# Optimization experiments

Measured on AMD Instinct MI355X. Metric: run time of the kernel, lower is better.

The kernel has to match this reference:

```python
import jax, jax.numpy as jnp
import numpy as np

D_MODEL = 1024
NUM_HEADS = 16
D_K = D_MODEL // NUM_HEADS
THETA = 10000.0


def setup_inputs() -> dict:
    key = jax.random.key(0)
    ks = jax.random.split(key, 5)
    B, S = 2, 2048
    sigma = np.sqrt(2.0 / (D_MODEL + D_MODEL))
    x = jax.random.normal(ks[0], (B, S, D_MODEL), dtype=jnp.float32)
    Wq = jax.random.normal(ks[1], (D_MODEL, D_MODEL), dtype=jnp.float32) * sigma
    Wk = jax.random.normal(ks[2], (D_MODEL, D_MODEL), dtype=jnp.float32) * sigma
    Wv = jax.random.normal(ks[3], (D_MODEL, D_MODEL), dtype=jnp.float32) * sigma
    Wo = jax.random.normal(ks[4], (D_MODEL, D_MODEL), dtype=jnp.float32) * sigma
    return {"x": x, "Wq": Wq, "Wk": Wk, "Wv": Wv, "Wo": Wo}


def _rope(x, cos, sin):
    # x: [B, H, S, D_K]; cos/sin: [S, D_K//2] broadcast to [1, 1, S, D_K//2]
    x1 = x[..., ::2]
    x2 = x[..., 1::2]
    even = x1 * cos - x2 * sin
    odd = x1 * sin + x2 * cos
    return jnp.stack((even, odd), axis=-1).reshape(x.shape)


def reference(x, Wq, Wk, Wv, Wo):
    B, S, _ = x.shape
    # projections: weight is (out, in), applied as einsum('oi,...i->...o')
    q = jnp.einsum('oi,bsi->bso', Wq, x).reshape(B, S, NUM_HEADS, D_K).transpose(0, 2, 1, 3)
    k = jnp.einsum('oi,bsi->bso', Wk, x).reshape(B, S, NUM_HEADS, D_K).transpose(0, 2, 1, 3)
    v = jnp.einsum('oi,bsi->bso', Wv, x).reshape(B, S, NUM_HEADS, D_K).transpose(0, 2, 1, 3)
    # RoPE tables (token_positions = arange(S))
    inv_freq = 1.0 / (THETA ** (jnp.arange(0, D_K, 2, dtype=jnp.float32) / D_K))
    t = jnp.arange(S, dtype=jnp.float32)
    freqs = t[:, None] * inv_freq[None, :]          # [S, D_K/2]
    cos = jnp.cos(freqs)[None, None]                # [1,1,S,D_K/2]
    sin = jnp.sin(freqs)[None, None]
    q = _rope(q, cos, sin)
    k = _rope(k, cos, sin)
    # causal attention, full materialized scores (faithful to source)
    scores = jnp.einsum('bhid,bhjd->bhij', q, k) / np.sqrt(D_K).astype(np.float32)
    causal = jnp.tril(jnp.ones((S, S), dtype=bool))
    scores = jnp.where(causal, scores, -jnp.inf)
    attn = jax.nn.softmax(scores, axis=-1)
    out = jnp.einsum('bhij,bhjd->bhid', attn, v)    # [B,H,S,D_K]
    out = out.transpose(0, 2, 1, 3).reshape(B, S, D_MODEL)
    return jnp.einsum('oi,bsi->bso', Wo, out)
```

## Files before the change

kernel.cpp:

```cpp
#include <hip/hip_runtime.h>

#define D_MODEL 1024
#define NUM_HEADS 16
#define SEQ 2048
#define BATCH 2

typedef __attribute__((ext_vector_type(8))) short bf16x8;
typedef __attribute__((ext_vector_type(4))) float f32x4;

__device__ __forceinline__ float bf2f(unsigned short u) {
    return __uint_as_float(((unsigned int)u) << 16);
}
__device__ __forceinline__ unsigned short f2bf(float f) {
    unsigned int u = __float_as_uint(f);
    return (unsigned short)((u + 0x7FFFu + ((u >> 16) & 1u)) >> 16);
}
__device__ __forceinline__ ushort4 pack4(float4 v) {
    return make_ushort4(f2bf(v.x), f2bf(v.y), f2bf(v.z), f2bf(v.w));
}

__device__ __forceinline__ void gload_lds16(const unsigned short* g, unsigned short* l) {
    __builtin_amdgcn_global_load_lds(
        (const __attribute__((address_space(1))) unsigned int*)g,
        (__attribute__((address_space(3))) unsigned int*)l,
        16, 0, 0);
}

__device__ __forceinline__ bf16x8 lds_read_swz(const unsigned short (*tile)[64], int row, int chunk) {
    const char* p = reinterpret_cast<const char*>(tile);
    return *reinterpret_cast<const bf16x8*>(p + row * 128 + (((chunk ^ (row & 7))) << 4));
}

__device__ __forceinline__ bf16x8 lds_read_swz32(const unsigned short (*tile)[32], int row, int chunk) {
    const char* p = reinterpret_cast<const char*>(tile);
    return *reinterpret_cast<const bf16x8*>(p + row * 64 + (((chunk ^ ((row >> 1) & 3))) << 4));
}

__device__ __forceinline__ bf16x8 lds_read_swz128(const unsigned short (*tile)[128], int row, int chunk) {
    const char* p = reinterpret_cast<const char*>(tile);
    return *reinterpret_cast<const bf16x8*>(p + row * 256 + (((chunk ^ (row & 15))) << 4));
}

__global__ __launch_bounds__(256) void conv_kernel(
    const float* __restrict__ src, unsigned short* __restrict__ dst, int n4)
{
    int i = blockIdx.x * 256 + threadIdx.x;
    if (i < n4) {
        float4 v = reinterpret_cast<const float4*>(src)[i];
        reinterpret_cast<ushort4*>(dst)[i] = pack4(v);
    }
}

__global__ __launch_bounds__(256) void conv4_kernel(
    const float* __restrict__ x, const float* __restrict__ Wq,
    const float* __restrict__ Wk, const float* __restrict__ Wv,
    const float* __restrict__ Wo,
    unsigned short* __restrict__ xb, unsigned short* __restrict__ w3bf,
    unsigned short* __restrict__ wob,
    float2* __restrict__ tab)
{
    int i = blockIdx.x * 256 + threadIdx.x;
    const int NW = (wob != nullptr) ? 2097152 : 1835008;
    if (i < NW) {
        const float* src;
        unsigned short* dst;
        int off;
        if (i < 1048576) {
            src = x; dst = xb; off = i;
        } else if (i < 1835008) {
            int j = i - 1048576;
            int which = j >> 18;
            off = j & 0x3FFFF;
            src = (which == 0) ? Wq : (which == 1) ? Wk : Wv;
            dst = w3bf + ((size_t)which << 20);
        } else {
            off = i - 1835008;
            src = Wo; dst = wob;
        }
        float4 v = reinterpret_cast<const float4*>(src)[off];
        reinterpret_cast<ushort4*>(dst)[off] = pack4(v);
    } else {
        int idx = i - NW;
        if (idx < 65536) {
            int s = idx >> 5, d2 = idx & 31;
            float inv = powf(10000.0f, -(float)d2 / 32.0f);
            float sn, cs;
            sincosf((float)s * inv, &sn, &cs);
            tab[idx] = make_float2(cs, sn);
        }
    }
}

__global__ __launch_bounds__(256) void qkv_mfma_kernel(
    const unsigned short* __restrict__ xb,
    const unsigned short* __restrict__ w3,
    const float2* __restrict__ tab,
    unsigned short* __restrict__ qb, unsigned short* __restrict__ kb,
    unsigned short* __restrict__ vt)
{
    const int lin = blockIdx.x;
    const int b = lin & 7;
    const int t = lin >> 3;
    const int which = t % 3;
    const int y = t / 3;
    const unsigned short* __restrict__ W = w3 + (size_t)which * 1048576;
    const int m0 = y * 128;
    const int n0g = b * 128;

    __shared__ __align__(16) unsigned short As[2][128][32];
    __shared__ __align__(16) unsigned short Bs[2][128][32];

    const int tid = threadIdx.x;
    const int w = tid >> 6;
    const int lane = tid & 63;
    const int quad = lane >> 4;
    const int c15 = lane & 15;
    const int qm = w >> 1, qn = w & 1;
    const int srow4 = lane >> 2;
    const int sch4 = lane & 3;

    auto stage = [&](int k0, int buf) {
#pragma unroll
        for (int i = 0; i < 2; i++) {
            const int row = i * 64 + w * 16 + srow4;
            const int ch = sch4 ^ ((row >> 1) & 3);
            gload_lds16(xb + (size_t)(m0 + row) * 1024 + k0 + ch * 8,
                        &As[buf][i * 64 + w * 16][0]);
            gload_lds16(W + (size_t)(n0g + row) * 1024 + k0 + ch * 8,
                        &Bs[buf][i * 64 + w * 16][0]);
        }
    };

    f32x4 acc[4][4];
#pragma unroll
    for (int mi = 0; mi < 4; mi++)
#pragma unroll
        for (int ni = 0; ni < 4; ni++) acc[mi][ni] = (f32x4){0.f, 0.f, 0.f, 0.f};

    stage(0, 0);
    for (int k0 = 0; k0 < 1024; k0 += 32) {
        const int cb = (k0 >> 5) & 1;
        __syncthreads();
        if (k0 < 992) stage(k0 + 32, cb ^ 1);

        bf16x8 af[4], bfr[4];
#pragma unroll
        for (int mi = 0; mi < 4; mi++)
            af[mi] = lds_read_swz32(As[cb], qm * 64 + mi * 16 + c15, quad);
#pragma unroll
        for (int ni = 0; ni < 4; ni++)
            bfr[ni] = lds_read_swz32(Bs[cb], qn * 64 + ni * 16 + c15, quad);
#pragma unroll
        for (int mi = 0; mi < 4; mi++)
#pragma unroll
            for (int ni = 0; ni < 4; ni++)
                acc[mi][ni] = __builtin_amdgcn_mfma_f32_16x16x32_bf16(af[mi], bfr[ni], acc[mi][ni], 0, 0, 0);
    }

    __syncthreads();
    unsigned short* stg = &As[0][0][0] + w * (16 * 72);
    const int hq = b * 2 + qn;
    unsigned short* outp = (which == 0) ? qb : kb;
    const int odd = c15 & 1;

#pragma unroll
    for (int mi = 0; mi < 4; mi++) {
#pragma unroll
        for (int r = 0; r < 4; r++) {
            int m = m0 + qm * 64 + mi * 16 + quad * 4 + r;
            int s = m & (SEQ - 1);
            const float2* trow = tab + (s << 5);
#pragma unroll
            for (int ni = 0; ni < 4; ni++) {
                float val = acc[mi][ni][r];
                float res;
                if (which < 2) {
                    float part = __shfl_xor(val, 1);
                    float2 cs = trow[(ni * 16 + c15) >> 1];
                    res = odd ? (part * cs.y + val * cs.x) : (val * cs.x - part * cs.y);
                } else {
                    res = val;
                }
                stg[(quad * 4 + r) * 72 + ni * 16 + c15] = f2bf(res);
            }
        }
        if (which < 2) {
            int row = lane >> 2;
            int ch = lane & 3;
            int m = m0 + qm * 64 + mi * 16 + row;
            int s = m & (SEQ - 1);
            int bb = m >> 11;
            size_t ob = (((size_t)bb * NUM_HEADS + hq) * SEQ + s) * 64 + ch * 16;
            uint4 v0 = *reinterpret_cast<const uint4*>(&stg[row * 72 + ch * 16]);
            uint4 v1 = *reinterpret_cast<const uint4*>(&stg[row * 72 + ch * 16 + 8]);
            *reinterpret_cast<uint4*>(&outp[ob]) = v0;
            *reinterpret_cast<uint4*>(&outp[ob + 8]) = v1;
        } else {
            int mbase = m0 + qm * 64 + mi * 16;
            int bb = mbase >> 11;
            int s_base = mbase & (SEQ - 1);
            unsigned short tmp[16];
#pragma unroll
            for (int sl = 0; sl < 16; sl++) tmp[sl] = stg[sl * 72 + lane];
            size_t ob = (((size_t)bb * NUM_HEADS + hq) * 64 + lane) * SEQ + s_base;
            *reinterpret_cast<uint4*>(&vt[ob])     = *reinterpret_cast<uint4*>(&tmp[0]);
            *reinterpret_cast<uint4*>(&vt[ob + 8]) = *reinterpret_cast<uint4*>(&tmp[8]);
        }
    }
}

__global__ __launch_bounds__(512, 4) void attn_kernel(
    const unsigned short* __restrict__ qb, const unsigned short* __restrict__ kb,
    const unsigned short* __restrict__ vt, unsigned short* __restrict__ ab)
{
    const int xpair = blockIdx.y;
    const int bh = blockIdx.x;
    const int b = bh >> 4, h = bh & 15;
    const size_t base = (size_t)bh * SEQ * 64;
    const size_t vbase = (size_t)bh * 64 * SEQ;
    const int tid = threadIdx.x;
    const int w = tid >> 6;
    const int grp = w >> 2;
    const int wa = w & 3;
    const int lane = tid & 63;
    const int quad = lane >> 4;
    const int c15 = lane & 15;
    const int srow8 = lane >> 3;
    const int sch = lane & 7;
    const int srow16 = lane >> 4;
    const int sch16 = lane & 15;
    const float C = 0.125f;

    __shared__ __align__(16) unsigned short Ks[2][128][64];
    __shared__ __align__(16) unsigned short Vs[2][64][128];
    float* exch = (float*)&Ks[0][0][0];
    float2* ml  = (float2*)((char*)&Ks[0][0][0] + 17152);
    unsigned short* ost = &Vs[0][0][0];

    auto stage = [&](int sj, int buf) {
        const int j0s = sj * 128;
#pragma unroll
        for (int i = 0; i < 2; i++) {
            const int krow = w * 16 + i * 8 + srow8;
            const int kch = sch ^ (krow & 7);
            gload_lds16(kb + base + (size_t)(j0s + krow) * 64 + kch * 8,
                        &Ks[buf][w * 16 + i * 8][0]);
            const int vrow = w * 8 + i * 4 + srow16;
            const int vch = sch16 ^ (vrow & 15);
            gload_lds16(vt + vbase + (size_t)vrow * SEQ + j0s + vch * 8,
                        &Vs[buf][w * 8 + i * 4][0]);
        }
    };

    for (int pass = 0; pass < 2; pass++) {
        const int it = pass ? xpair : (31 - xpair);
        const int i0 = it * 64;
        const int nj = (it >> 1) + 1;

        const int qrow = i0 + wa * 16 + c15;
        bf16x8 qf0 = *reinterpret_cast<const bf16x8*>(&qb[base + (size_t)qrow * 64 + quad * 8]);
        bf16x8 qf1 = *reinterpret_cast<const bf16x8*>(&qb[base + (size_t)qrow * 64 + 32 + quad * 8]);

        float m_st = -1e30f, l_st = 0.f;
        f32x4 Oc[4];
#pragma unroll
        for (int t = 0; t < 4; t++) Oc[t] = (f32x4){0.f, 0.f, 0.f, 0.f};

        __syncthreads();
        stage(0, 0);

        for (int sj = 0; sj < nj; sj++) {
            const int cb = sj & 1;
            __syncthreads();
            if (sj < nj - 1) stage(sj + 1, cb ^ 1);

            const int j0 = sj * 128 + grp * 64;
            if (j0 <= i0) {
                bf16x8 kc0[4], kc1[4];
#pragma unroll
                for (int t = 0; t < 4; t++) {
                    kc0[t] = lds_read_swz(Ks[cb], grp * 64 + t * 16 + c15, quad);
                    kc1[t] = lds_read_swz(Ks[cb], grp * 64 + t * 16 + c15, 4 + quad);
                }

                f32x4 sc[4];
#pragma unroll
                for (int t = 0; t < 4; t++) sc[t] = (f32x4){0.f, 0.f, 0.f, 0.f};
                __builtin_amdgcn_s_setprio(1);
#pragma unroll
                for (int t = 0; t < 4; t++) {
                    sc[t] = __builtin_amdgcn_mfma_f32_16x16x32_bf16(kc0[t], qf0, sc[t], 0, 0, 0);
                    sc[t] = __builtin_amdgcn_mfma_f32_16x16x32_bf16(kc1[t], qf1, sc[t], 0, 0, 0);
                }
                __builtin_amdgcn_s_setprio(0);

                bf16x8 vv0[4], vv1[4];
#pragma unroll
                for (int t = 0; t < 4; t++) {
                    vv0[t] = lds_read_swz128(Vs[cb], t * 16 + c15, grp * 8 + quad);
                    vv1[t] = lds_read_swz128(Vs[cb], t * 16 + c15, grp * 8 + 4 + quad);
                }

                if (j0 == i0) {
                    const int gi = i0 + wa * 16 + c15;
#pragma unroll
                    for (int t = 0; t < 4; t++) {
#pragma unroll
                        for (int r = 0; r < 4; r++) {
                            int gj = j0 + t * 16 + quad * 4 + r;
                            if (gj > gi) sc[t][r] = -1e30f;
                        }
                    }
                }

                float x0 = fmaxf(fmaxf(sc[0][0], sc[0][1]), fmaxf(sc[0][2], sc[0][3]));
                float x1 = fmaxf(fmaxf(sc[1][0], sc[1][1]), fmaxf(sc[1][2], sc[1][3]));
                float x2 = fmaxf(fmaxf(sc[2][0], sc[2][1]), fmaxf(sc[2][2], sc[2][3]));
                float x3 = fmaxf(fmaxf(sc[3][0], sc[3][1]), fmaxf(sc[3][2], sc[3][3]));
                float tm = fmaxf(fmaxf(x0, x1), fmaxf(x2, x3));
                tm = fmaxf(tm, __shfl_xor(tm, 16));
                tm = fmaxf(tm, __shfl_xor(tm, 32));

                if (!__all(tm <= m_st + 64.0f)) {
                    float mnew = fmaxf(m_st, tm);
                    float alpha = __expf((m_st - mnew) * C);
                    l_st *= alpha;
#pragma unroll
                    for (int t = 0; t < 4; t++)
#pragma unroll
                        for (int r = 0; r < 4; r++) Oc[t][r] *= alpha;
                    m_st = mnew;
                }

                const float mC = m_st * C;
                float p[4][4];
#pragma unroll
                for (int t = 0; t < 4; t++)
#pragma unroll
                    for (int r = 0; r < 4; r++)
                        p[t][r] = __expf(__builtin_fmaf(sc[t][r], C, -mC));

                float s0 = (p[0][0] + p[0][1]) + (p[0][2] + p[0][3]);
                float s1 = (p[1][0] + p[1][1]) + (p[1][2] + p[1][3]);
                float s2 = (p[2][0] + p[2][1]) + (p[2][2] + p[2][3]);
                float s3 = (p[3][0] + p[3][1]) + (p[3][2] + p[3][3]);
                l_st += (s0 + s1) + (s2 + s3);

                unsigned int pk[4][2];
#pragma unroll
                for (int t = 0; t < 4; t++)
#pragma unroll
                    for (int hh = 0; hh < 2; hh++)
                        asm("v_cvt_pk_bf16_f32 %0, %1, %2"
                            : "=v"(pk[t][hh]) : "v"(p[t][2 * hh]), "v"(p[t][2 * hh + 1]));

                unsigned int w0[4], w1[4];
#pragma unroll
                for (int e = 0; e < 4; e++) {
                    int sl = c15 + 16 * ((2 * quad + (e >> 1)) & 3);
                    unsigned int a0 = (unsigned int)__shfl((int)pk[0][e & 1], sl);
                    unsigned int b0 = (unsigned int)__shfl((int)pk[1][e & 1], sl);
                    w0[e] = (quad >> 1) ? b0 : a0;
                    unsigned int a1 = (unsigned int)__shfl((int)pk[2][e & 1], sl);
                    unsigned int b1 = (unsigned int)__shfl((int)pk[3][e & 1], sl);
                    w1[e] = (quad >> 1) ? b1 : a1;
                }
                uint4 u0 = make_uint4(w0[0], w0[1], w0[2], w0[3]);
                uint4 u1 = make_uint4(w1[0], w1[1], w1[2], w1[3]);
                bf16x8 ap0 = *reinterpret_cast<bf16x8*>(&u0);
                bf16x8 ap1 = *reinterpret_cast<bf16x8*>(&u1);

                __builtin_amdgcn_s_setprio(1);
#pragma unroll
                for (int t = 0; t < 4; t++) {
                    Oc[t] = __builtin_amdgcn_mfma_f32_16x16x32_bf16(vv0[t], ap0, Oc[t], 0, 0, 0);
                    Oc[t] = __builtin_amdgcn_mfma_f32_16x16x32_bf16(vv1[t], ap1, Oc[t], 0, 0, 0);
                }
                __builtin_amdgcn_s_setprio(0);
            }
        }

        __syncthreads();
        float l_row = l_st;
        l_row += __shfl_xor(l_row, 16);
        l_row += __shfl_xor(l_row, 32);
        const int q = wa * 16 + c15;

        if (grp == 1) {
#pragma unroll
            for (int t = 0; t < 4; t++)
#pragma unroll
                for (int r = 0; r < 4; r++)
                    exch[q * 65 + t * 16 + quad * 4 + r] = Oc[t][r];
            if (quad == 0) ml[q] = make_float2(m_st, l_row);
        }
        __syncthreads();
        if (grp == 0) {
            float2 mlB = ml[q];
            float m = fmaxf(m_st, mlB.x);
            float aA = __expf((m_st - m) * C);
            float aB = __expf((mlB.x - m) * C);
            float inv = 1.0f / (l_row * aA + mlB.y * aB);
#pragma unroll
            for (int t = 0; t < 4; t++) {
#pragma unroll
                for (int hh = 0; hh < 2; hh++) {
                    float o0 = (Oc[t][2 * hh] * aA
                                + exch[q * 65 + t * 16 + quad * 4 + 2 * hh] * aB) * inv;
                    float o1 = (Oc[t][2 * hh + 1] * aA
                                + exch[q * 65 + t * 16 + quad * 4 + 2 * hh + 1] * aB) * inv;
                    unsigned int pko = (unsigned int)f2bf(o0) | ((unsigned int)f2bf(o1) << 16);
                    *reinterpret_cast<unsigned int*>(
                        &ost[q * 72 + t * 16 + quad * 4 + 2 * hh]) = pko;
                }
            }
            {
                int row = lane >> 2;
                int ch = lane & 3;
                int gi = i0 + wa * 16 + row;
                size_t ob = ((size_t)b * SEQ + gi) * 1024 + h * 64 + ch * 16;
                uint4 v0 = *reinterpret_cast<const uint4*>(&ost[(wa * 16 + row) * 72 + ch * 16]);
                uint4 v1 = *reinterpret_cast<const uint4*>(&ost[(wa * 16 + row) * 72 + ch * 16 + 8]);
                *reinterpret_cast<uint4*>(&ab[ob]) = v0;
                *reinterpret_cast<uint4*>(&ab[ob + 8]) = v1;
            }
        }
    }
}

__global__ __launch_bounds__(256) void out_mfma_kernel(
    const unsigned short* __restrict__ A, const unsigned short* __restrict__ Wob,
    float* __restrict__ out)
{
    const int lin = blockIdx.x;
    const int b = lin & 7;
    const int y = lin >> 3;
    const int m0 = y * 64;
    const int n0g = b * 128;

    __shared__ __align__(16) unsigned short As[2][64][32];
    __shared__ __align__(16) unsigned short Bs[2][128][32];

    const int tid = threadIdx.x;
    const int w = tid >> 6;
    const int lane = tid & 63;
    const int quad = lane >> 4;
    const int c15 = lane & 15;
    const int qm = w >> 1, qn = w & 1;
    const int srow4 = lane >> 2;
    const int sch4 = lane & 3;

    auto stage = [&](int k0, int buf) {
        {
            const int row = w * 16 + srow4;
            const int ch = sch4 ^ ((row >> 1) & 3);
            gload_lds16(A + (size_t)(m0 + row) * 1024 + k0 + ch * 8,
                        &As[buf][w * 16][0]);
        }
#pragma unroll
        for (int i = 0; i < 2; i++) {
            const int row = i * 64 + w * 16 + srow4;
            const int ch = sch4 ^ ((row >> 1) & 3);
            gload_lds16(Wob + (size_t)(n0g + row) * 1024 + k0 + ch * 8,
                        &Bs[buf][i * 64 + w * 16][0]);
        }
    };

    f32x4 acc[2][4];
#pragma unroll
    for (int mi = 0; mi < 2; mi++)
#pragma unroll
        for (int ni = 0; ni < 4; ni++) acc[mi][ni] = (f32x4){0.f, 0.f, 0.f, 0.f};

    stage(0, 0);
    for (int k0 = 0; k0 < 1024; k0 += 32) {
        const int cb = (k0 >> 5) & 1;
        __syncthreads();
        if (k0 < 992) stage(k0 + 32, cb ^ 1);

        bf16x8 af[2], bfr[4];
#pragma unroll
        for (int mi = 0; mi < 2; mi++)
            af[mi] = lds_read_swz32(As[cb], qm * 32 + mi * 16 + c15, quad);
#pragma unroll
        for (int ni = 0; ni < 4; ni++)
            bfr[ni] = lds_read_swz32(Bs[cb], qn * 64 + ni * 16 + c15, quad);
#pragma unroll
        for (int mi = 0; mi < 2; mi++)
#pragma unroll
            for (int ni = 0; ni < 4; ni++)
                acc[mi][ni] = __builtin_amdgcn_mfma_f32_16x16x32_bf16(af[mi], bfr[ni], acc[mi][ni], 0, 0, 0);
    }

#pragma unroll
    for (int mi = 0; mi < 2; mi++) {
#pragma unroll
        for (int r = 0; r < 4; r++) {
            int m = m0 + qm * 32 + mi * 16 + quad * 4 + r;
#pragma unroll
            for (int ni = 0; ni < 4; ni++) {
                int n = n0g + qn * 64 + ni * 16 + c15;
                out[(size_t)m * 1024 + n] = acc[mi][ni][r];
            }
        }
    }
}

extern "C" void kernel_launch(void* const* d_in, const int* in_sizes, int n_in,
                              void* d_out, int out_size, void* d_ws, size_t ws_size,
                              hipStream_t stream)
{
    const float* x  = (const float*)d_in[0];
    const float* Wq = (const float*)d_in[1];
    const float* Wk = (const float*)d_in[2];
    const float* Wv = (const float*)d_in[3];
    const float* Wo = (const float*)d_in[4];
    float* out = (float*)d_out;

    const size_t QKV_ELEMS = (size_t)BATCH * SEQ * D_MODEL;

    unsigned short* qb = (unsigned short*)d_ws;
    unsigned short* kb = qb + QKV_ELEMS;
    unsigned short* vt = kb + QKV_ELEMS;
    unsigned short* ab = vt + QKV_ELEMS;
    unsigned short* w3bf = ab;
    unsigned short* xbuf = (unsigned short*)d_out;
    float2* tab = (float2*)((char*)d_out + 8 * 1024 * 1024);

    const size_t used = 4 * QKV_ELEMS * sizeof(unsigned short);
    const size_t wo_bytes = 1048576 * sizeof(unsigned short);
    if (ws_size >= used + wo_bytes) {
        unsigned short* wobf = qb + 4 * QKV_ELEMS;
        conv4_kernel<<<dim3(8448), 256, 0, stream>>>(x, Wq, Wk, Wv, Wo,
                                                     xbuf, w3bf, wobf, tab);
        qkv_mfma_kernel<<<dim3(768), 256, 0, stream>>>(xbuf, w3bf, tab, qb, kb, vt);
        attn_kernel<<<dim3(32, 16), 512, 0, stream>>>(qb, kb, vt, ab);
        out_mfma_kernel<<<dim3(512), 256, 0, stream>>>(ab, wobf, out);
    } else {
        unsigned short* wobf = qb;
        conv4_kernel<<<dim3(7424), 256, 0, stream>>>(x, Wq, Wk, Wv, Wo,
                                                     xbuf, w3bf, nullptr, tab);
        qkv_mfma_kernel<<<dim3(768), 256, 0, stream>>>(xbuf, w3bf, tab, qb, kb, vt);
        attn_kernel<<<dim3(32, 16), 512, 0, stream>>>(qb, kb, vt, ab);
        conv_kernel<<<dim3(1024), 256, 0, stream>>>(Wo, wobf, 262144);
        out_mfma_kernel<<<dim3(512), 256, 0, stream>>>(ab, wobf, out);
    }
}
```

Baseline: 194.8 us.

## Software-pipeline PV matmul one tile behind QK softmax with triple-buffered V

Defers each tile's P·V MFMA to the next loop iteration so it overlaps with the next tile's QK^T MFMAs and softmax exp work. V gets a third LDS buffer so the pending tile's V stays valid while the next tile is staged. The output rescale by alpha is also deferred and applied just before the pending PV. The cost is more LDS, more live registers (the pending P fragments, alpha and the flag) and an epilogue that drains the last pending tile.

Result: no change. 196.4 us (+0.8%).

```diff
diff --git a/kernel.cpp b/kernel.cpp
--- a/kernel.cpp
+++ b/kernel.cpp
@@ -232,23 +232,24 @@
     const float C = 0.125f;
 
     __shared__ __align__(16) unsigned short Ks[2][128][64];
-    __shared__ __align__(16) unsigned short Vs[2][64][128];
+    __shared__ __align__(16) unsigned short Vs[3][64][128];
     float* exch = (float*)&Ks[0][0][0];
     float2* ml  = (float2*)((char*)&Ks[0][0][0] + 17152);
     unsigned short* ost = &Vs[0][0][0];
 
-    auto stage = [&](int sj, int buf) {
+    auto stage = [&](int sj) {
         const int j0s = sj * 128;
+        const int kbuf = sj & 1, vbuf = sj % 3;
 #pragma unroll
         for (int i = 0; i < 2; i++) {
             const int krow = w * 16 + i * 8 + srow8;
             const int kch = sch ^ (krow & 7);
             gload_lds16(kb + base + (size_t)(j0s + krow) * 64 + kch * 8,
-                        &Ks[buf][w * 16 + i * 8][0]);
+                        &Ks[kbuf][w * 16 + i * 8][0]);
             const int vrow = w * 8 + i * 4 + srow16;
             const int vch = sch16 ^ (vrow & 15);
             gload_lds16(vt + vbase + (size_t)vrow * SEQ + j0s + vch * 8,
-                        &Vs[buf][w * 8 + i * 4][0]);
+                        &Vs[vbuf][w * 8 + i * 4][0]);
         }
     };
 
@@ -261,123 +262,174 @@
         bf16x8 qf0 = *reinterpret_cast<const bf16x8*>(&qb[base + (size_t)qrow * 64 + quad * 8]);
         bf16x8 qf1 = *reinterpret_cast<const bf16x8*>(&qb[base + (size_t)qrow * 64 + 32 + quad * 8]);
 
-        float m_st = -1e30f, l_st = 0.f;
-        f32x4 Oc[4];
-#pragma unroll
-        for (int t = 0; t < 4; t++) Oc[t] = (f32x4){0.f, 0.f, 0.f, 0.f};
+        float m_st = -1e30f, l_st = 0.f, alpha_p = 1.f;
+        int pend = -1;
+        bool resc_p = false;
+        bf16x8 ap0, ap1;
+        f32x4 Oc0 = (f32x4){0.f,0.f,0.f,0.f}, Oc1 = Oc0, Oc2 = Oc0, Oc3 = Oc0;
 
         __syncthreads();
-        stage(0, 0);
+        stage(0);
 
         for (int sj = 0; sj < nj; sj++) {
-            const int cb = sj & 1;
             __syncthreads();
-            if (sj < nj - 1) stage(sj + 1, cb ^ 1);
+            if (sj + 1 < nj) stage(sj + 1);
 
             const int j0 = sj * 128 + grp * 64;
-            if (j0 <= i0) {
-                bf16x8 kc0[4], kc1[4];
-#pragma unroll
-                for (int t = 0; t < 4; t++) {
-                    kc0[t] = lds_read_swz(Ks[cb], grp * 64 + t * 16 + c15, quad);
-                    kc1[t] = lds_read_swz(Ks[cb], grp * 64 + t * 16 + c15, 4 + quad);
-                }
-
-                f32x4 sc[4];
-#pragma unroll
-                for (int t = 0; t < 4; t++) sc[t] = (f32x4){0.f, 0.f, 0.f, 0.f};
+            const bool act = (j0 <= i0);
+
+            f32x4 sc0, sc1, sc2, sc3;
+            if (act) {
+                const unsigned short (*Kt)[64] = Ks[sj & 1];
+                bf16x8 k00 = lds_read_swz(Kt, grp * 64 +  0 + c15, quad);
+                bf16x8 k01 = lds_read_swz(Kt, grp * 64 + 16 + c15, quad);
+                bf16x8 k02 = lds_read_swz(Kt, grp * 64 + 32 + c15, quad);
+                bf16x8 k03 = lds_read_swz(Kt, grp * 64 + 48 + c15, quad);
+                bf16x8 k10 = lds_read_swz(Kt, grp * 64 +  0 + c15, 4 + quad);
+                bf16x8 k11 = lds_read_swz(Kt, grp * 64 + 16 + c15, 4 + quad);
+                bf16x8 k12 = lds_read_swz(Kt, grp * 64 + 32 + c15, 4 + quad);
+                bf16x8 k13 = lds_read_swz(Kt, grp * 64 + 48 + c15, 4 + quad);
+                f32x4 z = (f32x4){0.f,0.f,0.f,0.f};
                 __builtin_amdgcn_s_setprio(1);
-#pragma unroll
-                for (int t = 0; t < 4; t++) {
-                    sc[t] = __builtin_amdgcn_mfma_f32_16x16x32_bf16(kc0[t], qf0, sc[t], 0, 0, 0);
-                    sc[t] = __builtin_amdgcn_mfma_f32_16x16x32_bf16(kc1[t], qf1, sc[t], 0, 0, 0);
-                }
+                sc0 = __builtin_amdgcn_mfma_f32_16x16x32_bf16(k00, qf0, z, 0, 0, 0);
+                sc1 = __builtin_amdgcn_mfma_f32_16x16x32_bf16(k01, qf0, z, 0, 0, 0);
+                sc2 = __builtin_amdgcn_mfma_f32_16x16x32_bf16(k02, qf0, z, 0, 0, 0);
+                sc3 = __builtin_amdgcn_mfma_f32_16x16x32_bf16(k03, qf0, z, 0, 0, 0);
+                sc0 = __builtin_amdgcn_mfma_f32_16x16x32_bf16(k10, qf1, sc0, 0, 0, 0);
+                sc1 = __builtin_amdgcn_mfma_f32_16x16x32_bf16(k11, qf1, sc1, 0, 0, 0);
+                sc2 = __builtin_amdgcn_mfma_f32_16x16x32_bf16(k12, qf1, sc2, 0, 0, 0);
+                sc3 = __builtin_amdgcn_mfma_f32_16x16x32_bf16(k13, qf1, sc3, 0, 0, 0);
                 __builtin_amdgcn_s_setprio(0);
-
-                bf16x8 vv0[4], vv1[4];
-#pragma unroll
-                for (int t = 0; t < 4; t++) {
-                    vv0[t] = lds_read_swz128(Vs[cb], t * 16 + c15, grp * 8 + quad);
-                    vv1[t] = lds_read_swz128(Vs[cb], t * 16 + c15, grp * 8 + 4 + quad);
-                }
-
+            }
+
+            if (pend >= 0) {
+                const unsigned short (*Vt)[128] = Vs[pend % 3];
+                bf16x8 v00 = lds_read_swz128(Vt,  0 + c15, grp * 8 + quad);
+                bf16x8 v01 = lds_read_swz128(Vt, 16 + c15, grp * 8 + quad);
+                bf16x8 v02 = lds_read_swz128(Vt, 32 + c15, grp * 8 + quad);
+                bf16x8 v03 = lds_read_swz128(Vt, 48 + c15, grp * 8 + quad);
+                bf16x8 v10 = lds_read_swz128(Vt,  0 + c15, grp * 8 + 4 + quad);
+                bf16x8 v11 = lds_read_swz128(Vt, 16 + c15, grp * 8 + 4 + quad);
+                bf16x8 v12 = lds_read_swz128(Vt, 32 + c15, grp * 8 + 4 + quad);
+                bf16x8 v13 = lds_read_swz128(Vt, 48 + c15, grp * 8 + 4 + quad);
+                if (resc_p) {
+#pragma unroll
+                    for (int r = 0; r < 4; r++) {
+                        Oc0[r] *= alpha_p; Oc1[r] *= alpha_p;
+                        Oc2[r] *= alpha_p; Oc3[r] *= alpha_p;
+                    }
+                    resc_p = false;
+                }
+                __builtin_amdgcn_s_setprio(1);
+                Oc0 = __builtin_amdgcn_mfma_f32_16x16x32_bf16(v00, ap0, Oc0, 0, 0, 0);
+                Oc1 = __builtin_amdgcn_mfma_f32_16x16x32_bf16(v01, ap0, Oc1, 0, 0, 0);
+                Oc2 = __builtin_amdgcn_mfma_f32_16x16x32_bf16(v02, ap0, Oc2, 0, 0, 0);
+                Oc3 = __builtin_amdgcn_mfma_f32_16x16x32_bf16(v03, ap0, Oc3, 0, 0, 0);
+                Oc0 = __builtin_amdgcn_mfma_f32_16x16x32_bf16(v10, ap1, Oc0, 0, 0, 0);
+                Oc1 = __builtin_amdgcn_mfma_f32_16x16x32_bf16(v11, ap1, Oc1, 0, 0, 0);
+                Oc2 = __builtin_amdgcn_mfma_f32_16x16x32_bf16(v12, ap1, Oc2, 0, 0, 0);
+                Oc3 = __builtin_amdgcn_mfma_f32_16x16x32_bf16(v13, ap1, Oc3, 0, 0, 0);
+                __builtin_amdgcn_s_setprio(0);
+                pend = -1;
+            }
+
+            if (act) {
                 if (j0 == i0) {
                     const int gi = i0 + wa * 16 + c15;
 #pragma unroll
-                    for (int t = 0; t < 4; t++) {
-#pragma unroll
-                        for (int r = 0; r < 4; r++) {
-                            int gj = j0 + t * 16 + quad * 4 + r;
-                            if (gj > gi) sc[t][r] = -1e30f;
-                        }
+                    for (int r = 0; r < 4; r++) {
+                        if (j0 +  0 + quad * 4 + r > gi) sc0[r] = -1e30f;
+                        if (j0 + 16 + quad * 4 + r > gi) sc1[r] = -1e30f;
+                        if (j0 + 32 + quad * 4 + r > gi) sc2[r] = -1e30f;
+                        if (j0 + 48 + quad * 4 + r > gi) sc3[r] = -1e30f;
                     }
                 }
-
-                float x0 = fmaxf(fmaxf(sc[0][0], sc[0][1]), fmaxf(sc[0][2], sc[0][3]));
-                float x1 = fmaxf(fmaxf(sc[1][0], sc[1][1]), fmaxf(sc[1][2], sc[1][3]));
-                float x2 = fmaxf(fmaxf(sc[2][0], sc[2][1]), fmaxf(sc[2][2], sc[2][3]));
-                float x3 = fmaxf(fmaxf(sc[3][0], sc[3][1]), fmaxf(sc[3][2], sc[3][3]));
+                float x0 = fmaxf(fmaxf(sc0[0], sc0[1]), fmaxf(sc0[2], sc0[3]));
+                float x1 = fmaxf(fmaxf(sc1[0], sc1[1]), fmaxf(sc1[2], sc1[3]));
+                float x2 = fmaxf(fmaxf(sc2[0], sc2[1]), fmaxf(sc2[2], sc2[3]));
+                float x3 = fmaxf(fmaxf(sc3[0], sc3[1]), fmaxf(sc3[2], sc3[3]));
                 float tm = fmaxf(fmaxf(x0, x1), fmaxf(x2, x3));
                 tm = fmaxf(tm, __shfl_xor(tm, 16));
                 tm = fmaxf(tm, __shfl_xor(tm, 32));
 
                 if (!__all(tm <= m_st + 64.0f)) {
                     float mnew = fmaxf(m_st, tm);
-                    float alpha = __expf((m_st - mnew) * C);
-                    l_st *= alpha;
-#pragma unroll
-                    for (int t = 0; t < 4; t++)
-#pragma unroll
-                        for (int r = 0; r < 4; r++) Oc[t][r] *= alpha;
+                    alpha_p = __expf((m_st - mnew) * C);
+                    l_st *= alpha_p;
                     m_st = mnew;
+                    resc_p = true;
                 }
 
                 const float mC = m_st * C;
-                float p[4][4];
-#pragma unroll
-                for (int t = 0; t < 4; t++)
-#pragma unroll
-                    for (int r = 0; r < 4; r++)
-                        p[t][r] = __expf(__builtin_fmaf(sc[t][r], C, -mC));
-
-                float s0 = (p[0][0] + p[0][1]) + (p[0][2] + p[0][3]);
-                float s1 = (p[1][0] + p[1][1]) + (p[1][2] + p[1][3]);
-                float s2 = (p[2][0] + p[2][1]) + (p[2][2] + p[2][3]);
-                float s3 = (p[3][0] + p[3][1]) + (p[3][2] + p[3][3]);
-                l_st += (s0 + s1) + (s2 + s3);
-
-                unsigned int pk[4][2];
-#pragma unroll
-                for (int t = 0; t < 4; t++)
-#pragma unroll
-                    for (int hh = 0; hh < 2; hh++)
-                        asm("v_cvt_pk_bf16_f32 %0, %1, %2"
-                            : "=v"(pk[t][hh]) : "v"(p[t][2 * hh]), "v"(p[t][2 * hh + 1]));
-
-                unsigned int w0[4], w1[4];
+                float p0[4], p1[4], p2[4], p3[4];
+#pragma unroll
+                for (int r = 0; r < 4; r++) {
+                    p0[r] = __expf(__builtin_fmaf(sc0[r], C, -mC));
+                    p1[r] = __expf(__builtin_fmaf(sc1[r], C, -mC));
+                    p2[r] = __expf(__builtin_fmaf(sc2[r], C, -mC));
+                    p3[r] = __expf(__builtin_fmaf(sc3[r], C, -mC));
+                }
+                l_st += ((p0[0]+p0[1])+(p0[2]+p0[3])) + ((p1[0]+p1[1])+(p1[2]+p1[3]))
+                      + ((p2[0]+p2[1])+(p2[2]+p2[3])) + ((p3[0]+p3[1])+(p3[2]+p3[3]));
+
+                unsigned int pk00, pk01, pk10, pk11, pk20, pk21, pk30, pk31;
+                asm("v_cvt_pk_bf16_f32 %0, %1, %2" : "=v"(pk00) : "v"(p0[0]), "v"(p0[1]));
+                asm("v_cvt_pk_bf16_f32 %0, %1, %2" : "=v"(pk01) : "v"(p0[2]), "v"(p0[3]));
+                asm("v_cvt_pk_bf16_f32 %0, %1, %2" : "=v"(pk10) : "v"(p1[0]), "v"(p1[1]));
+                asm("v_cvt_pk_bf16_f32 %0, %1, %2" : "=v"(pk11) : "v"(p1[2]), "v"(p1[3]));
+                asm("v_cvt_pk_bf16_f32 %0, %1, %2" : "=v"(pk20) : "v"(p2[0]), "v"(p2[1]));
+                asm("v_cvt_pk_bf16_f32 %0, %1, %2" : "=v"(pk21) : "v"(p2[2]), "v"(p2[3]));
+                asm("v_cvt_pk_bf16_f32 %0, %1, %2" : "=v"(pk30) : "v"(p3[0]), "v"(p3[1]));
+                asm("v_cvt_pk_bf16_f32 %0, %1, %2" : "=v"(pk31) : "v"(p3[2]), "v"(p3[3]));
+
+                unsigned int w00, w01, w02, w03, w10, w11, w12, w13;
 #pragma unroll
                 for (int e = 0; e < 4; e++) {
                     int sl = c15 + 16 * ((2 * quad + (e >> 1)) & 3);
-                    unsigned int a0 = (unsigned int)__shfl((int)pk[0][e & 1], sl);
-                    unsigned int b0 = (unsigned int)__shfl((int)pk[1][e & 1], sl);
-                    w0[e] = (quad >> 1) ? b0 : a0;
-                    unsigned int a1 = (unsigned int)__shfl((int)pk[2][e & 1], sl);
-                    unsigned int b1 = (unsigned int)__shfl((int)pk[3][e & 1], sl);
-                    w1[e] = (quad >> 1) ? b1 : a1;
-                }
-                uint4 u0 = make_uint4(w0[0], w0[1], w0[2], w0[3]);
-                uint4 u1 = make_uint4(w1[0], w1[1], w1[2], w1[3]);
-                bf16x8 ap0 = *reinterpret_cast<bf16x8*>(&u0);
-                bf16x8 ap1 = *reinterpret_cast<bf16x8*>(&u1);
-
-                __builtin_amdgcn_s_setprio(1);
-#pragma unroll
-                for (int t = 0; t < 4; t++) {
-                    Oc[t] = __builtin_amdgcn_mfma_f32_16x16x32_bf16(vv0[t], ap0, Oc[t], 0, 0, 0);
-                    Oc[t] = __builtin_amdgcn_mfma_f32_16x16x32_bf16(vv1[t], ap1, Oc[t], 0, 0, 0);
-                }
-                __builtin_amdgcn_s_setprio(0);
-            }
+                    unsigned int a0 = (unsigned int)__shfl((int)((e & 1) ? pk01 : pk00), sl);
+                    unsigned int b0 = (unsigned int)__shfl((int)((e & 1) ? pk11 : pk10), sl);
+                    unsigned int r0 = (quad >> 1) ? b0 : a0;
+                    unsigned int a1 = (unsigned int)__shfl((int)((e & 1) ? pk21 : pk20), sl);
+                    unsigned int b1 = (unsigned int)__shfl((int)((e & 1) ? pk31 : pk30), sl);
+                    unsigned int r1 = (quad >> 1) ? b1 : a1;
+                    if (e == 0) { w00 = r0; w10 = r1; }
+                    else if (e == 1) { w01 = r0; w11 = r1; }
+                    else if (e == 2) { w02 = r0; w12 = r1; }
+                    else { w03 = r0; w13 = r1; }
+                }
+                uint4 u0 = make_uint4(w00, w01, w02, w03);
+                uint4 u1 = make_uint4(w10, w11, w12, w13);
+                ap0 = *reinterpret_cast<bf16x8*>(&u0);
+                ap1 = *reinterpret_cast<bf16x8*>(&u1);
+                pend = sj;
+            }
+        }
+
+        if (pend >= 0) {
+            const unsigned short (*Vt)[128] = Vs[pend % 3];
+            bf16x8 v00 = lds_read_swz128(Vt,  0 + c15, grp * 8 + quad);
+            bf16x8 v01 = lds_read_swz128(Vt, 16 + c15, grp * 8 + quad);
+            bf16x8 v02 = lds_read_swz128(Vt, 32 + c15, grp * 8 + quad);
+            bf16x8 v03 = lds_read_swz128(Vt, 48 + c15, grp * 8 + quad);
+            bf16x8 v10 = lds_read_swz128(Vt,  0 + c15, grp * 8 + 4 + quad);
+            bf16x8 v11 = lds_read_swz128(Vt, 16 + c15, grp * 8 + 4 + quad);
+            bf16x8 v12 = lds_read_swz128(Vt, 32 + c15, grp * 8 + 4 + quad);
+            bf16x8 v13 = lds_read_swz128(Vt, 48 + c15, grp * 8 + 4 + quad);
+            if (resc_p) {
+#pragma unroll
+                for (int r = 0; r < 4; r++) {
+                    Oc0[r] *= alpha_p; Oc1[r] *= alpha_p;
+                    Oc2[r] *= alpha_p; Oc3[r] *= alpha_p;
+                }
+            }
+            Oc0 = __builtin_amdgcn_mfma_f32_16x16x32_bf16(v00, ap0, Oc0, 0, 0, 0);
+            Oc1 = __builtin_amdgcn_mfma_f32_16x16x32_bf16(v01, ap0, Oc1, 0, 0, 0);
+            Oc2 = __builtin_amdgcn_mfma_f32_16x16x32_bf16(v02, ap0, Oc2, 0, 0, 0);
+            Oc3 = __builtin_amdgcn_mfma_f32_16x16x32_bf16(v03, ap0, Oc3, 0, 0, 0);
+            Oc0 = __builtin_amdgcn_mfma_f32_16x16x32_bf16(v10, ap1, Oc0, 0, 0, 0);
+            Oc1 = __builtin_amdgcn_mfma_f32_16x16x32_bf16(v11, ap1, Oc1, 0, 0, 0);
+            Oc2 = __builtin_amdgcn_mfma_f32_16x16x32_bf16(v12, ap1, Oc2, 0, 0, 0);
+            Oc3 = __builtin_amdgcn_mfma_f32_16x16x32_bf16(v13, ap1, Oc3, 0, 0, 0);
         }
 
         __syncthreads();
@@ -388,10 +440,12 @@
 
         if (grp == 1) {
 #pragma unroll
-            for (int t = 0; t < 4; t++)
-#pragma unroll
-                for (int r = 0; r < 4; r++)
-                    exch[q * 65 + t * 16 + quad * 4 + r] = Oc[t][r];
+            for (int r = 0; r < 4; r++) {
+                exch[q * 65 +  0 + quad * 4 + r] = Oc0[r];
+                exch[q * 65 + 16 + quad * 4 + r] = Oc1[r];
+                exch[q * 65 + 32 + quad * 4 + r] = Oc2[r];
+                exch[q * 65 + 48 + quad * 4 + r] = Oc3[r];
+            }
             if (quad == 0) ml[q] = make_float2(m_st, l_row);
         }
         __syncthreads();
@@ -403,11 +457,12 @@
             float inv = 1.0f / (l_row * aA + mlB.y * aB);
 #pragma unroll
             for (int t = 0; t < 4; t++) {
+                f32x4 Ot = (t == 0) ? Oc0 : (t == 1) ? Oc1 : (t == 2) ? Oc2 : Oc3;
 #pragma unroll
                 for (int hh = 0; hh < 2; hh++) {
-                    float o0 = (Oc[t][2 * hh] * aA
+                    float o0 = (Ot[2 * hh] * aA
                                 + exch[q * 65 + t * 16 + quad * 4 + 2 * hh] * aB) * inv;
-                    float o1 = (Oc[t][2 * hh + 1] * aA
+                    float o1 = (Ot[2 * hh + 1] * aA
                                 + exch[q * 65 + t * 16 + quad * 4 + 2 * hh + 1] * aB) * inv;
                     unsigned int pko = (unsigned int)f2bf(o0) | ((unsigned int)f2bf(o1) << 16);
                     *reinterpret_cast<unsigned int*>(
```
